# Performance work log

Measured on AMD Instinct MI355X. Metric: run time of the kernel, lower is better.

## Reference

```python
import jax, jax.numpy as jnp
import numpy as np

EPS = 1e-10

def _normalize(v):
    # v: (..., 3); matches torch v / (norm(v) + 1e-10)
    n = jnp.sqrt(jnp.sum(v * v, axis=-1, keepdims=True))
    return v / (n + EPS)

def setup_inputs() -> dict:
    key = jax.random.key(0)
    N = 4_000_000
    coords = jax.random.normal(key, (N, 3), dtype=jnp.float32)
    return {"coords": coords}

def reference(coords):
    n = coords.shape[0]
    d = coords[1:] - coords[:-1]          # (n-1, 3) consecutive differences
    v1 = _normalize(d[:-1])               # (n-2, 3)  coords[i]-coords[i-1], i=1..n-2
    v2 = _normalize(d[1:])                # (n-2, 3)  coords[i+1]-coords[i]

    # torsion angles: same acos(clamp(dot)) broadcast to 3 columns
    cos_angle = jnp.clip(jnp.sum(v1 * v2, axis=-1), -1.0, 1.0)  # (n-2,)
    angle = jnp.arccos(cos_angle)
    angles = jnp.zeros((n, 3), dtype=coords.dtype)
    angles = angles.at[1:-1].set(angle[:, None])

    # local frames: Gram-Schmidt on (v1, v2) plus cross product
    e1 = v1
    proj = jnp.sum(v2 * e1, axis=-1, keepdims=True)
    e2 = _normalize(v2 - proj * e1)
    e3 = jnp.cross(e1, e2)
    frames_mid = jnp.stack([e1, e2, e3], axis=1)  # (n-2, 3, 3) rows are e1,e2,e3
    frames = jnp.zeros((n, 3, 3), dtype=coords.dtype)
    frames = frames.at[1:-1].set(frames_mid)
    frames = frames.at[0].set(frames[1])
    frames = frames.at[-1].set(frames[-2])

    return angles, frames
```

## Files before the change

kernel.cpp:

```cpp
#include <hip/hip_runtime.h>
#include <math.h>

#define TPB 256

__global__ __launch_bounds__(TPB) void geo_kernel(const float* __restrict__ coords,
                                                  float* __restrict__ out, int n) {
    __shared__ float s_ang[TPB * 3];
    __shared__ float s_frm[TPB * 9];

    const int tid  = threadIdx.x;
    const int base = blockIdx.x * TPB;
    const int r    = base + tid;

    if (r < n) {
        int rr = r;
        if (rr < 1) rr = 1;
        if (rr > n - 2) rr = n - 2;

        const float* p = coords + 3 * (size_t)(rr - 1);
        float ax = p[0], ay = p[1], az = p[2];
        float bx = p[3], by = p[4], bz = p[5];
        float cx = p[6], cy = p[7], cz = p[8];

        float d1x = bx - ax, d1y = by - ay, d1z = bz - az;
        float d2x = cx - bx, d2y = cy - by, d2z = cz - bz;

        float n1   = sqrtf(d1x * d1x + d1y * d1y + d1z * d1z) + 1e-10f;
        float inv1 = 1.0f / n1;
        float v1x = d1x * inv1, v1y = d1y * inv1, v1z = d1z * inv1;

        float n2   = sqrtf(d2x * d2x + d2y * d2y + d2z * d2z) + 1e-10f;
        float inv2 = 1.0f / n2;
        float v2x = d2x * inv2, v2y = d2y * inv2, v2z = d2z * inv2;

        float dotv   = v1x * v2x + v1y * v2y + v1z * v2z;
        float cosang = fminf(1.0f, fmaxf(-1.0f, dotv));
        float ang    = (r == 0 || r == n - 1) ? 0.0f : acosf(cosang);

        float tx = v2x - dotv * v1x, ty = v2y - dotv * v1y, tz = v2z - dotv * v1z;
        float tn   = sqrtf(tx * tx + ty * ty + tz * tz) + 1e-10f;
        float invt = 1.0f / tn;
        float e2x = tx * invt, e2y = ty * invt, e2z = tz * invt;

        float e3x = v1y * e2z - v1z * e2y;
        float e3y = v1z * e2x - v1x * e2z;
        float e3z = v1x * e2y - v1y * e2x;

        s_ang[tid * 3 + 0] = ang;
        s_ang[tid * 3 + 1] = ang;
        s_ang[tid * 3 + 2] = ang;

        float* f = s_frm + tid * 9;
        f[0] = v1x; f[1] = v1y; f[2] = v1z;
        f[3] = e2x; f[4] = e2y; f[5] = e2z;
        f[6] = e3x; f[7] = e3y; f[8] = e3z;
    }
    __syncthreads();

    float* angles = out;
    float* frames = out + (size_t)n * 3;

    int valid = n - base;
    if (valid > TPB) valid = TPB;

    if (valid == TPB) {
        float4*       ga = (float4*)(angles + (size_t)base * 3);
        const float4* sa = (const float4*)s_ang;
        if (tid < (TPB * 3) / 4) ga[tid] = sa[tid];

        float4*       gf = (float4*)(frames + (size_t)base * 9);
        const float4* sf = (const float4*)s_frm;
        #pragma unroll
        for (int k = 0; k < (TPB * 9) / 4; k += TPB) {
            int idx = k + tid;
            if (idx < (TPB * 9) / 4) gf[idx] = sf[idx];
        }
    } else {
        if (r < n) {
            angles[(size_t)r * 3 + 0] = s_ang[tid * 3 + 0];
            angles[(size_t)r * 3 + 1] = s_ang[tid * 3 + 1];
            angles[(size_t)r * 3 + 2] = s_ang[tid * 3 + 2];
            for (int k = 0; k < 9; ++k)
                frames[(size_t)r * 9 + k] = s_frm[tid * 9 + k];
        }
    }
}

extern "C" void kernel_launch(void* const* d_in, const int* in_sizes, int n_in,
                              void* d_out, int out_size, void* d_ws, size_t ws_size,
                              hipStream_t stream) {
    const float* coords = (const float*)d_in[0];
    float*       out    = (float*)d_out;
    int n = in_sizes[0] / 3;
    int blocks = (n + TPB - 1) / TPB;
    hipLaunchKernelGGL(geo_kernel, dim3(blocks), dim3(TPB), 0, stream, coords, out, n);
}
```

Baseline: 219.9 us.

## Stage coords in LDS with float4 loads, share normalized diffs, nontemporal stores

Each block now loads its coordinate window plus halo into shared memory with coalesced float4 loads. It computes each normalized difference vector once into shared memory, so two threads no longer redo the same normalization, and it drops the scattered 9-float per-thread global reads. Output writes use nontemporal stores to avoid polluting the cache. The cost is two extra barriers and more LDS use per block, which may lower occupancy.

Measured after the change: 217.4 us. About the same (-1.1%).

```diff
diff --git a/kernel.cpp b/kernel.cpp
--- a/kernel.cpp
+++ b/kernel.cpp
@@ -3,43 +3,70 @@
 
 #define TPB 256
 
+typedef float f32x4 __attribute__((ext_vector_type(4)));
+
 __global__ __launch_bounds__(TPB) void geo_kernel(const float* __restrict__ coords,
                                                   float* __restrict__ out, int n) {
+    __shared__ float s_crd[780];
+    __shared__ float s_v[258 * 3];
     __shared__ float s_ang[TPB * 3];
     __shared__ float s_frm[TPB * 9];
 
-    const int tid  = threadIdx.x;
-    const int base = blockIdx.x * TPB;
-    const int r    = base + tid;
+    const int  tid  = threadIdx.x;
+    const int  base = blockIdx.x * TPB;
+    const int  r    = base + tid;
+    const long n3   = (long)n * 3;
+    const long g0   = (long)base * 3;
+
+    {
+        const long gs = g0 - 8;
+        if (tid < 195) {
+            long gf = gs + 4 * (long)tid;
+            float4 val;
+            if (gf >= 0 && gf + 4 <= n3) {
+                val = *(const float4*)(coords + gf);
+            } else {
+                val.x = (gf + 0 >= 0 && gf + 0 < n3) ? coords[gf + 0] : 0.0f;
+                val.y = (gf + 1 >= 0 && gf + 1 < n3) ? coords[gf + 1] : 0.0f;
+                val.z = (gf + 2 >= 0 && gf + 2 < n3) ? coords[gf + 2] : 0.0f;
+                val.w = (gf + 3 >= 0 && gf + 3 < n3) ? coords[gf + 3] : 0.0f;
+            }
+            *(float4*)(s_crd + 4 * tid) = val;
+        }
+    }
+    __syncthreads();
+
+    for (int t = tid; t < 258; t += TPB) {
+        long vi = (long)base - 2 + t;
+        if (vi >= 0 && vi <= (long)n - 2) {
+            const float* c0 = s_crd + 2 + 3 * t;
+            float dx = c0[3] - c0[0];
+            float dy = c0[4] - c0[1];
+            float dz = c0[5] - c0[2];
+            float inv = 1.0f / (sqrtf(dx * dx + dy * dy + dz * dz) + 1e-10f);
+            s_v[3 * t + 0] = dx * inv;
+            s_v[3 * t + 1] = dy * inv;
+            s_v[3 * t + 2] = dz * inv;
+        }
+    }
+    __syncthreads();
 
     if (r < n) {
         int rr = r;
         if (rr < 1) rr = 1;
         if (rr > n - 2) rr = n - 2;
 
-        const float* p = coords + 3 * (size_t)(rr - 1);
-        float ax = p[0], ay = p[1], az = p[2];
-        float bx = p[3], by = p[4], bz = p[5];
-        float cx = p[6], cy = p[7], cz = p[8];
-
-        float d1x = bx - ax, d1y = by - ay, d1z = bz - az;
-        float d2x = cx - bx, d2y = cy - by, d2z = cz - bz;
-
-        float n1   = sqrtf(d1x * d1x + d1y * d1y + d1z * d1z) + 1e-10f;
-        float inv1 = 1.0f / n1;
-        float v1x = d1x * inv1, v1y = d1y * inv1, v1z = d1z * inv1;
-
-        float n2   = sqrtf(d2x * d2x + d2y * d2y + d2z * d2z) + 1e-10f;
-        float inv2 = 1.0f / n2;
-        float v2x = d2x * inv2, v2y = d2y * inv2, v2z = d2z * inv2;
+        const int lv = rr - base + 1;
+        const float* pv = s_v + 3 * lv;
+        float v1x = pv[0], v1y = pv[1], v1z = pv[2];
+        float v2x = pv[3], v2y = pv[4], v2z = pv[5];
 
         float dotv   = v1x * v2x + v1y * v2y + v1z * v2z;
         float cosang = fminf(1.0f, fmaxf(-1.0f, dotv));
         float ang    = (r == 0 || r == n - 1) ? 0.0f : acosf(cosang);
 
         float tx = v2x - dotv * v1x, ty = v2y - dotv * v1y, tz = v2z - dotv * v1z;
-        float tn   = sqrtf(tx * tx + ty * ty + tz * tz) + 1e-10f;
-        float invt = 1.0f / tn;
+        float invt = 1.0f / (sqrtf(tx * tx + ty * ty + tz * tz) + 1e-10f);
         float e2x = tx * invt, e2y = ty * invt, e2z = tz * invt;
 
         float e3x = v1y * e2z - v1z * e2y;
@@ -64,16 +91,18 @@
     if (valid > TPB) valid = TPB;
 
     if (valid == TPB) {
-        float4*       ga = (float4*)(angles + (size_t)base * 3);
-        const float4* sa = (const float4*)s_ang;
-        if (tid < (TPB * 3) / 4) ga[tid] = sa[tid];
+        f32x4*       ga = (f32x4*)(angles + (size_t)base * 3);
+        const f32x4* sa = (const f32x4*)s_ang;
+        if (tid < (TPB * 3) / 4)
+            __builtin_nontemporal_store(sa[tid], &ga[tid]);
 
-        float4*       gf = (float4*)(frames + (size_t)base * 9);
-        const float4* sf = (const float4*)s_frm;
+        f32x4*       gf = (f32x4*)(frames + (size_t)base * 9);
+        const f32x4* sf = (const f32x4*)s_frm;
         #pragma unroll
         for (int k = 0; k < (TPB * 9) / 4; k += TPB) {
             int idx = k + tid;
-            if (idx < (TPB * 9) / 4) gf[idx] = sf[idx];
+            if (idx < (TPB * 9) / 4)
+                __builtin_nontemporal_store(sf[idx], &gf[idx]);
         }
     } else {
         if (r < n) {
```
